# Optimization experiments

Measured on AMD Instinct MI355X. Metric: run time of the kernel, lower is better.

## Reference

```python
import jax, jax.numpy as jnp
import numpy as np

N, T, J, NB = 2048, 81, 16, 15
D_ATT, HEADS, SEQ, D_LIN, NOISE = 48, 6, 31, 256, 45
BN_EPS, LN_EPS, SLOPE = 1e-5, 1e-6, 0.01

# Human3.6M 16-joint skeleton bone (parent, child) pairs
_BONES = [(0,1),(1,2),(2,3),(0,4),(4,5),(5,6),(0,7),(7,8),(8,9),(9,10),(8,11),(11,12),(12,13),(8,14),(14,15)]
BONES_P = np.array([p for p, c in _BONES])
BONES_C = np.array([c for p, c in _BONES])
_parent = {c: p for p, c in _BONES}
_bone_of = {c: i for i, (p, c) in enumerate(_BONES)}
_M = np.zeros((NB, J), np.float32)  # M[i,j]=1 iff bone i lies on root->joint j chain
for j in range(1, J):
    jj = j
    while jj != 0:
        _M[_bone_of[jj], j] = 1.0
        jj = _parent[jj]
M_BONE2POSE = jnp.asarray(_M)
FIXED_MASK = jnp.ones((NB,), jnp.float32).at[jnp.array([6, 7])].set(0.0)  # torso bones kept fixed


def _layer_norm(t, a, b):
    mean = t.mean(-1, keepdims=True)
    # torch.std default is unbiased (ddof=1); module divides by (std + eps)
    std = jnp.sqrt(((t - mean) ** 2).sum(-1, keepdims=True) / (t.shape[-1] - 1))
    return a * (t - mean) / (std + LN_EPS) + b


def _leaky(x):
    return jnp.where(x >= 0, x, SLOPE * x)


def _axis_angle_to_matrix(v):
    # Rodrigues: v (..., 3) axis-angle -> (..., 3, 3)
    theta = jnp.linalg.norm(v, axis=-1, keepdims=True)
    k = v / jnp.maximum(theta, 1e-8)
    c = jnp.cos(theta)[..., None]
    s = jnp.sin(theta)[..., None]
    kx, ky, kz = k[..., 0], k[..., 1], k[..., 2]
    z = jnp.zeros_like(kx)
    K = jnp.stack([jnp.stack([z, -kz, ky], -1),
                   jnp.stack([kz, z, -kx], -1),
                   jnp.stack([-ky, kx, z], -1)], -2)
    kk = k[..., :, None] * k[..., None, :]
    return c * jnp.eye(3, dtype=v.dtype) + s * K + (1 - c) * kk


def setup_inputs() -> dict:
    key = jax.random.key(0)
    ks = jax.random.split(key, 12)
    w = lambda k, shape, scale=0.05: jax.random.normal(k, shape, jnp.float32) * scale
    return {
        'inputs_3d': jax.random.normal(ks[0], (N, 1, T, J, 3), jnp.float32),
        'noise': jax.random.normal(ks[1], (N, NOISE), jnp.float32),
        'enc_w': w(ks[2], (D_ATT, 3)), 'enc_b': jnp.zeros((D_ATT,), jnp.float32),
        'enc_bn_g': jnp.ones((D_ATT,), jnp.float32), 'enc_bn_b': jnp.zeros((D_ATT,), jnp.float32),
        'ln_a': jnp.ones((D_ATT,), jnp.float32), 'ln_b': jnp.zeros((D_ATT,), jnp.float32),
        'wq': w(ks[3], (D_ATT, D_ATT)), 'bq': jnp.zeros((D_ATT,), jnp.float32),
        'wk': w(ks[4], (D_ATT, D_ATT)), 'bk': jnp.zeros((D_ATT,), jnp.float32),
        'wv': w(ks[5], (D_ATT, D_ATT)), 'bv': jnp.zeros((D_ATT,), jnp.float32),
        'wo': w(ks[6], (D_ATT, D_ATT)), 'bo': jnp.zeros((D_ATT,), jnp.float32),
        'w1': w(ks[7], (D_LIN, SEQ * D_ATT)), 'b1': jnp.zeros((D_LIN,), jnp.float32),
        'bn1_g': jnp.ones((D_LIN,), jnp.float32), 'bn1_b': jnp.zeros((D_LIN,), jnp.float32),
        'w2': w(ks[8], (NB * 4, D_LIN)), 'b2': w(ks[9], (NB * 4,), 0.1),
    }


def reference(inputs_3d, noise, enc_w, enc_b, enc_bn_g, enc_bn_b, ln_a, ln_b,
              wq, bq, wk, bk, wv, bv, wo, bo, w1, b1, bn1_g, bn1_b, w2, b2):
    x5 = inputs_3d[:, 0]                                  # (n, T, 16, 3)
    root = x5[:, :, :1, :]
    x = x5 - root                                         # root-centered
    bvec = x[..., BONES_C, :] - x[..., BONES_P, :]        # (n, T, 15, 3)
    blen = jnp.linalg.norm(bvec, axis=-1, keepdims=True)
    bunit = bvec / blen
    n, t_len = x.shape[0], x.shape[1]
    mid = (t_len - 1) // 2

    x_ = x[:, mid].reshape(n, -1)                         # (n, 48)
    y = jnp.concatenate([x_, noise], axis=-1).reshape(n, SEQ, 3)
    # Conv1d(k=1) == per-token linear; BatchNorm eval (running mean 0, var 1); Dropout off
    y = jax.nn.relu((y @ enc_w.T + enc_b) * enc_bn_g / jnp.sqrt(1.0 + BN_EPS) + enc_bn_b)

    # tiny 6-head self-attention with pre-LayerNorm and residual
    h = _layer_norm(y, ln_a, ln_b)
    d = D_ATT // HEADS
    q = (h @ wq.T + bq).reshape(n, SEQ, HEADS, d).transpose(0, 2, 1, 3)
    k = (h @ wk.T + bk).reshape(n, SEQ, HEADS, d).transpose(0, 2, 1, 3)
    v = (h @ wv.T + bv).reshape(n, SEQ, HEADS, d).transpose(0, 2, 1, 3)
    probs = jax.nn.softmax(jnp.einsum('nhqd,nhkd->nhqk', q, k) / (d ** 0.5), axis=-1)
    ctx = jnp.einsum('nhqk,nhkd->nhqd', probs, v).transpose(0, 2, 1, 3).reshape(n, SEQ, D_ATT)
    y = y + (ctx @ wo.T + bo)

    y = y.reshape(n, -1)                                  # (n, 1488)
    y = _leaky((y @ w1.T + b1) * bn1_g / jnp.sqrt(1.0 + BN_EPS) + bn1_b)
    y = _leaky(y @ w2.T + b2).reshape(n, NB, 4)           # (n, 15, 4)

    axis = y[..., :3]
    axis = axis / jnp.linalg.norm(axis, axis=-1, keepdims=True)
    theta = y[..., 3:4] / t_len                           # (n, 15, 1)
    t_idx = jnp.arange(t_len, dtype=y.dtype)              # (T,)
    vaa = axis[:, None] * (theta[:, None] * t_idx[None, :, None, None])  # (n, T, 15, 3)
    R = _axis_angle_to_matrix(vaa)                        # (n, T, 15, 3, 3)
    mod_unit = jnp.einsum('ntbij,ntbj->ntbi', R, bunit)
    mask = FIXED_MASK[None, None, :, None]
    mod_unit = mod_unit * mask + bunit * (1 - mask)
    ba_diff = 1 - jnp.sum(mod_unit * bunit, axis=-1)      # (n, T, 15)
    mod_bone = mod_unit * blen
    out = jnp.einsum('ntbc,bj->ntjc', mod_bone, M_BONE2POSE) + root  # (n, T, 16, 3)
    return out, ba_diff
```

## Files before the change

kernel.cpp:

```cpp
#include <hip/hip_runtime.h>
#include <math.h>

#define NS   2048
#define TL   81
#define NBN  15
#define DA   48
#define SQL  31
#define KD   1488
#define DL   256
#define MID  40
#define SWLD 52

#define INV_SQRT_BN 0.99999500003749969f
#define SCALE_ATT   0.35355339059327373f

__global__ __launch_bounds__(256)
void attn_kernel(const float* __restrict__ x5, const float* __restrict__ noise,
                 const float* __restrict__ enc_w, const float* __restrict__ enc_b,
                 const float* __restrict__ enc_g, const float* __restrict__ enc_bb,
                 const float* __restrict__ ln_a, const float* __restrict__ ln_b,
                 const float* __restrict__ wq, const float* __restrict__ bq,
                 const float* __restrict__ wk, const float* __restrict__ bk,
                 const float* __restrict__ wv, const float* __restrict__ bv,
                 const float* __restrict__ wo, const float* __restrict__ bo,
                 float* __restrict__ y2)
{
    __shared__ float s93[96];
    __shared__ __align__(16) float sy[32*SWLD];
    __shared__ __align__(16) float sh[32*SWLD];
    __shared__ __align__(16) float sW[3*48*SWLD];
    __shared__ __align__(16) float sQKV[32*148];
    __shared__ float smean[32], sinv[32];

    const int tid = threadIdx.x;
    const int n = blockIdx.x;

    if (tid < 93) {
        float v;
        if (tid < 48) {
            const float* base = x5 + ((size_t)n*TL + MID)*48;
            v = base[tid] - base[tid % 3];
        } else {
            v = noise[(size_t)n*45 + (tid-48)];
        }
        s93[tid] = v;
    }
    #pragma unroll
    for (int l=0; l<9; l++){
        int idx = tid + l*256;
        int f = idx/48, c = idx - f*48;
        int o = f*SWLD + c;
        sW[o]             = wq[idx];
        sW[48*SWLD  + o]  = wk[idx];
        sW[96*SWLD  + o]  = wv[idx];
    }
    __syncthreads();

    for (int idx=tid; idx<SQL*DA; idx+=256){
        int s = idx/48, f = idx - s*48;
        float a = enc_b[f]
                + s93[s*3+0]*enc_w[f*3+0]
                + s93[s*3+1]*enc_w[f*3+1]
                + s93[s*3+2]*enc_w[f*3+2];
        float v = a * (enc_g[f]*INV_SQRT_BN) + enc_bb[f];
        sy[s*SWLD+f] = fmaxf(v, 0.0f);
    }
    __syncthreads();

    if (tid < SQL){
        float m = 0.f;
        for (int f=0; f<48; f++) m += sy[tid*SWLD+f];
        m *= (1.0f/48.0f);
        float vs = 0.f;
        for (int f=0; f<48; f++){ float d = sy[tid*SWLD+f]-m; vs += d*d; }
        float sd = sqrtf(vs * (1.0f/47.0f));
        smean[tid] = m;
        sinv[tid]  = 1.0f/(sd + 1e-6f);
    }
    __syncthreads();

    for (int idx=tid; idx<SQL*DA; idx+=256){
        int s = idx/48, f = idx - s*48;
        sh[s*SWLD+f] = ln_a[f]*(sy[s*SWLD+f]-smean[s])*sinv[s] + ln_b[f];
    }
    __syncthreads();

    if (tid < 192){
        const int sg  = tid/24;
        const int rem = tid - sg*24;
        const int arr = rem >> 3;
        const int fg  = rem & 7;
        const int f0  = fg*6;
        const int s0  = sg*4;
        const float* wb = sW + arr*48*SWLD + f0*SWLD;
        const float* hb = sh + s0*SWLD;
        float acc[4][6];
        #pragma unroll
        for (int j=0;j<4;j++)
            #pragma unroll
            for (int i=0;i<6;i++) acc[j][i]=0.f;
        for (int cc=0; cc<12; cc++){
            const int c0 = 4*((fg + cc) % 12);
            float4 h0 = *(const float4*)(hb + 0*SWLD + c0);
            float4 h1 = *(const float4*)(hb + 1*SWLD + c0);
            float4 h2 = *(const float4*)(hb + 2*SWLD + c0);
            float4 h3 = *(const float4*)(hb + 3*SWLD + c0);
            #pragma unroll
            for (int i=0;i<6;i++){
                float4 w = *(const float4*)(wb + i*SWLD + c0);
                acc[0][i] += h0.x*w.x + h0.y*w.y + h0.z*w.z + h0.w*w.w;
                acc[1][i] += h1.x*w.x + h1.y*w.y + h1.z*w.z + h1.w*w.w;
                acc[2][i] += h2.x*w.x + h2.y*w.y + h2.z*w.z + h2.w*w.w;
                acc[3][i] += h3.x*w.x + h3.y*w.y + h3.z*w.z + h3.w*w.w;
            }
        }
        const float* bias = (arr==0)? bq : (arr==1? bk : bv);
        #pragma unroll
        for (int i=0;i<6;i++){
            float b = bias[f0+i];
            int col = arr*48 + f0 + i;
            sQKV[(s0+0)*148 + col] = acc[0][i] + b;
            sQKV[(s0+1)*148 + col] = acc[1][i] + b;
            sQKV[(s0+2)*148 + col] = acc[2][i] + b;
            sQKV[(s0+3)*148 + col] = acc[3][i] + b;
        }
    }
    __syncthreads();

    #pragma unroll
    for (int l=0; l<9; l++){
        int idx = tid + l*256;
        sW[(idx/48)*SWLD + (idx%48)] = wo[idx];
    }
    if (tid < 186){
        const int hd = tid/31, qi = tid - (tid/31)*31;
        const float4 q0 = *(const float4*)(sQKV + qi*148 + hd*8);
        const float4 q1 = *(const float4*)(sQKV + qi*148 + hd*8 + 4);
        float sc[31]; float mx = -1e30f;
        for (int ki=0; ki<31; ki++){
            const float4 k0 = *(const float4*)(sQKV + ki*148 + 48 + hd*8);
            const float4 k1 = *(const float4*)(sQKV + ki*148 + 48 + hd*8 + 4);
            float d = q0.x*k0.x + q0.y*k0.y + q0.z*k0.z + q0.w*k0.w
                    + q1.x*k1.x + q1.y*k1.y + q1.z*k1.z + q1.w*k1.w;
            d *= SCALE_ATT;
            sc[ki] = d; mx = fmaxf(mx, d);
        }
        float ssum = 0.f;
        for (int ki=0; ki<31; ki++){ float e = expf(sc[ki]-mx); sc[ki]=e; ssum += e; }
        float rin = 1.0f/ssum;
        float4 c0 = {0,0,0,0}, c1 = {0,0,0,0};
        for (int ki=0; ki<31; ki++){
            float p = sc[ki];
            const float4 v0 = *(const float4*)(sQKV + ki*148 + 96 + hd*8);
            const float4 v1 = *(const float4*)(sQKV + ki*148 + 96 + hd*8 + 4);
            c0.x += p*v0.x; c0.y += p*v0.y; c0.z += p*v0.z; c0.w += p*v0.w;
            c1.x += p*v1.x; c1.y += p*v1.y; c1.z += p*v1.z; c1.w += p*v1.w;
        }
        float* cb = sh + qi*SWLD + hd*8;
        float4 o0, o1;
        o0.x=c0.x*rin; o0.y=c0.y*rin; o0.z=c0.z*rin; o0.w=c0.w*rin;
        o1.x=c1.x*rin; o1.y=c1.y*rin; o1.z=c1.z*rin; o1.w=c1.w*rin;
        *(float4*)(cb)   = o0;
        *(float4*)(cb+4) = o1;
    }
    __syncthreads();

    if (tid < 192){
        const int sg = tid/12;
        const int fg = tid - sg*12;
        const int f0 = fg*4;
        const float* wb = sW + f0*SWLD;
        const float* cb = sh + sg*2*SWLD;
        float a0[4]={0,0,0,0}, a1[4]={0,0,0,0};
        for (int cc=0; cc<12; cc++){
            const int c0 = 4*((fg + cc) % 12);
            float4 x0 = *(const float4*)(cb + c0);
            float4 x1 = *(const float4*)(cb + SWLD + c0);
            #pragma unroll
            for (int i=0;i<4;i++){
                float4 w = *(const float4*)(wb + i*SWLD + c0);
                a0[i] += x0.x*w.x + x0.y*w.y + x0.z*w.z + x0.w*w.w;
                a1[i] += x1.x*w.x + x1.y*w.y + x1.z*w.z + x1.w*w.w;
            }
        }
        {
            int s = sg*2;
            if (s < 31){
                float* dst = y2 + (size_t)n*KD + s*48 + f0;
                const float* yb = sy + s*SWLD + f0;
                #pragma unroll
                for (int i=0;i<4;i++) dst[i] = yb[i] + a0[i] + bo[f0+i];
            }
        }
        {
            int s = sg*2+1;
            if (s < 31){
                float* dst = y2 + (size_t)n*KD + s*48 + f0;
                const float* yb = sy + s*SWLD + f0;
                #pragma unroll
                for (int i=0;i<4;i++) dst[i] = yb[i] + a1[i] + bo[f0+i];
            }
        }
    }
}

#define KSP 6
#define KPS 248
#define KCH 8

__global__ __launch_bounds__(256)
void gemm1_kernel(const float* __restrict__ y2, const float* __restrict__ w1,
                  float* __restrict__ y3p)
{
    __shared__ __align__(16) float sB[KCH*256];
    __shared__ __align__(16) float sA[KCH*20];
    const int tid = threadIdx.x;
    const int bx = blockIdx.x;
    const int m0 = (bx & 127) * 16;
    const int split = bx >> 7;
    const int ks0 = split * KPS;
    const int c0 = (tid & 15)*4 + (tid >> 6)*64;
    const int r0 = ((tid >> 4) & 3)*4;

    const int bn = tid >> 1;
    const int bg = (tid & 1)*4;
    const int ar = tid >> 1;
    const int ag = (tid & 1)*4;

    float acc[4][4];
    #pragma unroll
    for (int i=0;i<4;i++)
        #pragma unroll
        for (int j=0;j<4;j++) acc[i][j]=0.f;

    for (int ch=0; ch<31; ch++){
        const int k0 = ks0 + ch*KCH;
        float4 b0v = *(const float4*)(w1 + (size_t)bn*KD        + k0 + bg);
        float4 b1v = *(const float4*)(w1 + (size_t)(bn+128)*KD  + k0 + bg);
        float4 av;
        if (tid < 32) av = *(const float4*)(y2 + (size_t)(m0+ar)*KD + k0 + ag);
        __syncthreads();
        sB[(bg+0)*256 + bn] = b0v.x;  sB[(bg+1)*256 + bn] = b0v.y;
        sB[(bg+2)*256 + bn] = b0v.z;  sB[(bg+3)*256 + bn] = b0v.w;
        sB[(bg+0)*256 + bn+128] = b1v.x;  sB[(bg+1)*256 + bn+128] = b1v.y;
        sB[(bg+2)*256 + bn+128] = b1v.z;  sB[(bg+3)*256 + bn+128] = b1v.w;
        if (tid < 32){
            sA[(ag+0)*20 + ar] = av.x;  sA[(ag+1)*20 + ar] = av.y;
            sA[(ag+2)*20 + ar] = av.z;  sA[(ag+3)*20 + ar] = av.w;
        }
        __syncthreads();
        #pragma unroll
        for (int kk=0; kk<KCH; kk++){
            float4 b = *(const float4*)(sB + kk*256 + c0);
            float4 a = *(const float4*)(sA + kk*20 + r0);
            acc[0][0] += a.x*b.x; acc[0][1] += a.x*b.y; acc[0][2] += a.x*b.z; acc[0][3] += a.x*b.w;
            acc[1][0] += a.y*b.x; acc[1][1] += a.y*b.y; acc[1][2] += a.y*b.z; acc[1][3] += a.y*b.w;
            acc[2][0] += a.z*b.x; acc[2][1] += a.z*b.y; acc[2][2] += a.z*b.z; acc[2][3] += a.z*b.w;
            acc[3][0] += a.w*b.x; acc[3][1] += a.w*b.y; acc[3][2] += a.w*b.z; acc[3][3] += a.w*b.w;
        }
    }

    float* dst = y3p + (size_t)split*NS*DL;
    #pragma unroll
    for (int i=0;i<4;i++){
        float4 v; v.x=acc[i][0]; v.y=acc[i][1]; v.z=acc[i][2]; v.w=acc[i][3];
        *(float4*)(dst + (size_t)(m0+r0+i)*DL + c0) = v;
    }
}

__global__ __launch_bounds__(256)
void head_kernel(const float* __restrict__ y3p, const float* __restrict__ w2,
                 const float* __restrict__ b2, const float* __restrict__ b1,
                 const float* __restrict__ g1, const float* __restrict__ bb1,
                 float* __restrict__ at)
{
    __shared__ float swc[64*60];
    __shared__ __align__(16) float sy3[8*256];
    __shared__ float sy4[8*61];
    const int tid = threadIdx.x;
    const int n0 = blockIdx.x * 8;

    #pragma unroll
    for (int l=0;l<2;l++){
        int idx = tid + l*256;
        int s = idx >> 6, i4 = (idx & 63) << 2;
        const float* src = y3p + (size_t)(n0+s)*256 + i4;
        float4 v = *(const float4*)(src);
        #pragma unroll
        for (int sl=1; sl<6; sl++){
            float4 p = *(const float4*)(src + (size_t)sl*NS*DL);
            v.x += p.x; v.y += p.y; v.z += p.z; v.w += p.w;
        }
        const float4 vb = *(const float4*)(b1 + i4);
        const float4 vg = *(const float4*)(g1 + i4);
        const float4 vs = *(const float4*)(bb1 + i4);
        v.x = (v.x + vb.x)*(vg.x*INV_SQRT_BN) + vs.x;  v.x = v.x>=0.f? v.x : 0.01f*v.x;
        v.y = (v.y + vb.y)*(vg.y*INV_SQRT_BN) + vs.y;  v.y = v.y>=0.f? v.y : 0.01f*v.y;
        v.z = (v.z + vb.z)*(vg.z*INV_SQRT_BN) + vs.z;  v.z = v.z>=0.f? v.z : 0.01f*v.z;
        v.w = (v.w + vb.w)*(vg.w*INV_SQRT_BN) + vs.w;  v.w = v.w>=0.f? v.w : 0.01f*v.w;
        *(float4*)(sy3 + s*256 + i4) = v;
    }

    float acc[2]; int ss[2], mm[2];
    #pragma unroll
    for (int l=0;l<2;l++){
        int uu = tid + l*256;
        ss[l]=0; mm[l]=0; acc[l]=0.f;
        if (uu < 480){ ss[l]=uu/60; mm[l]=uu-ss[l]*60; acc[l]=b2[mm[l]]; }
    }

    for (int ch=0; ch<4; ch++){
        const int i0 = ch*64;
        __syncthreads();
        #pragma unroll
        for (int l=0;l<15;l++){
            int idx = tid + l*256;
            int m = idx >> 6, io = idx & 63;
            swc[io*60 + m] = w2[(size_t)m*256 + i0 + io];
        }
        __syncthreads();
        #pragma unroll
        for (int l=0;l<2;l++){
            int uu = tid + l*256;
            if (uu < 480){
                const float* yy = sy3 + ss[l]*256 + i0;
                float a = acc[l];
                #pragma unroll 8
                for (int io=0; io<64; io++) a += yy[io]*swc[io*60 + mm[l]];
                acc[l] = a;
            }
        }
    }
    __syncthreads();
    #pragma unroll
    for (int l=0;l<2;l++){
        int uu = tid + l*256;
        if (uu < 480){
            float a = acc[l];
            sy4[ss[l]*61 + mm[l]] = a>=0.f? a : 0.01f*a;
        }
    }
    __syncthreads();
    if (tid < 120){
        int s = tid/15, b = tid - s*15;
        const float* y4 = sy4 + s*61 + b*4;
        float ax=y4[0], ay=y4[1], az=y4[2], th=y4[3];
        float nr = sqrtf(ax*ax+ay*ay+az*az);
        float4 o;
        o.x = ax/nr; o.y = ay/nr; o.z = az/nr; o.w = th/81.0f;
        *(float4*)(at + (size_t)(n0+s)*60 + b*4) = o;
    }
}

__global__ __launch_bounds__(256)
void pose_kernel(const float* __restrict__ x5, const float* __restrict__ at,
                 float* __restrict__ out)
{
    const int gid = blockIdx.x*256 + threadIdx.x;
    if (gid >= NS*TL) return;
    const int n = gid / TL;
    const int t = gid - n*TL;
    const float ft = (float)t;

    float4 pv[12];
    {
        const float4* src = (const float4*)(x5 + (size_t)gid*48);
        #pragma unroll
        for (int i=0;i<12;i++) pv[i] = src[i];
    }
    float* p = (float*)pv;
    const float4* ab = (const float4*)(at + (size_t)n*60);

    float4 posv[12];
    float* pos = (float*)posv;
    pos[0]=p[0]; pos[1]=p[1]; pos[2]=p[2];
    float ba[15];

    const int PJ[15] = {0,1,2,0,4,5,0,7,8,9,8,11,12,8,14};
    const int CJ[15] = {1,2,3,4,5,6,7,8,9,10,11,12,13,14,15};

    #pragma unroll
    for (int b=0;b<15;b++){
        const int pj = PJ[b], cj = CJ[b];
        float bx = p[cj*3+0]-p[pj*3+0];
        float by = p[cj*3+1]-p[pj*3+1];
        float bz = p[cj*3+2]-p[pj*3+2];
        float bl = sqrtf(bx*bx+by*by+bz*bz);
        float ux = bx/bl, uy = by/bl, uz = bz/bl;
        float mx, my, mz;
        if (b==6 || b==7){
            mx=ux; my=uy; mz=uz;
        } else {
            float4 a = ab[b];
            float ang = a.w * ft;
            float cs = __cosf(ang), sn = __sinf(ang);
            float kd = a.x*ux + a.y*uy + a.z*uz;
            float cx = a.y*uz - a.z*uy;
            float cy = a.z*ux - a.x*uz;
            float cz = a.x*uy - a.y*ux;
            float oc = (1.0f-cs)*kd;
            mx = ux*cs + cx*sn + a.x*oc;
            my = uy*cs + cy*sn + a.y*oc;
            mz = uz*cs + cz*sn + a.z*oc;
        }
        ba[b] = 1.0f - (mx*ux+my*uy+mz*uz);
        pos[cj*3+0] = pos[pj*3+0] + mx*bl;
        pos[cj*3+1] = pos[pj*3+1] + my*bl;
        pos[cj*3+2] = pos[pj*3+2] + mz*bl;
    }

    {
        float4* dst = (float4*)(out + (size_t)gid*48);
        #pragma unroll
        for (int i=0;i<12;i++) dst[i] = posv[i];
    }
    {
        float* bd = out + (size_t)NS*TL*48 + (size_t)gid*15;
        #pragma unroll
        for (int b=0;b<15;b++) bd[b] = ba[b];
    }
}

extern "C" void kernel_launch(void* const* d_in, const int* in_sizes, int n_in,
                              void* d_out, int out_size, void* d_ws, size_t ws_size,
                              hipStream_t stream)
{
    const float* x5    = (const float*)d_in[0];
    const float* noise = (const float*)d_in[1];
    const float* enc_w = (const float*)d_in[2];
    const float* enc_b = (const float*)d_in[3];
    const float* enc_g = (const float*)d_in[4];
    const float* enc_bb= (const float*)d_in[5];
    const float* ln_a  = (const float*)d_in[6];
    const float* ln_b  = (const float*)d_in[7];
    const float* wq = (const float*)d_in[8];
    const float* bq = (const float*)d_in[9];
    const float* wk = (const float*)d_in[10];
    const float* bk = (const float*)d_in[11];
    const float* wv = (const float*)d_in[12];
    const float* bv = (const float*)d_in[13];
    const float* wo = (const float*)d_in[14];
    const float* bo = (const float*)d_in[15];
    const float* w1 = (const float*)d_in[16];
    const float* b1 = (const float*)d_in[17];
    const float* g1 = (const float*)d_in[18];
    const float* bb1= (const float*)d_in[19];
    const float* w2 = (const float*)d_in[20];
    const float* b2 = (const float*)d_in[21];
    float* out = (float*)d_out;

    float* ws = (float*)d_ws;
    float* y2 = ws;
    float* at = y2 + (size_t)NS*KD;

    float* y3p = out;

    attn_kernel<<<NS, 256, 0, stream>>>(x5, noise, enc_w, enc_b, enc_g, enc_bb,
                                        ln_a, ln_b, wq,bq,wk,bk,wv,bv,wo,bo, y2);
    gemm1_kernel<<<128*KSP, 256, 0, stream>>>(y2, w1, y3p);
    head_kernel<<<NS/8, 256, 0, stream>>>(y3p, w2, b2, b1, g1, bb1, at);
    pose_kernel<<<(NS*TL+255)/256, 256, 0, stream>>>(x5, at, out);

    (void)in_sizes; (void)n_in; (void)out_size; (void)ws_size;
}
```

Before: 236.3 us.

## Drop shared-memory staging in gemm1; load A and B tiles directly per thread

The split-K GEMM no longer stages W1 and activation chunks through LDS with two barriers per chunk. Each thread now reads its own 4 rows of A and 4 rows of W1 straight from global memory as float4 and accumulates dot products in registers. This removes the barriers and LDS traffic but gives up cross-thread reuse: each W1 row is read by many threads, so the kernel leans on L1/L2 cache. The strided row access pattern also coalesces poorly within a wavefront.

Measured after the change: 307.5 us. 30.1% more time.

```diff
diff --git a/kernel.cpp b/kernel.cpp
--- a/kernel.cpp
+++ b/kernel.cpp
@@ -212,8 +212,6 @@
 void gemm1_kernel(const float* __restrict__ y2, const float* __restrict__ w1,
                   float* __restrict__ y3p)
 {
-    __shared__ __align__(16) float sB[KCH*256];
-    __shared__ __align__(16) float sA[KCH*20];
     const int tid = threadIdx.x;
     const int bx = blockIdx.x;
     const int m0 = (bx & 127) * 16;
@@ -222,10 +220,8 @@
     const int c0 = (tid & 15)*4 + (tid >> 6)*64;
     const int r0 = ((tid >> 4) & 3)*4;
 
-    const int bn = tid >> 1;
-    const int bg = (tid & 1)*4;
-    const int ar = tid >> 1;
-    const int ag = (tid & 1)*4;
+    const float* arow = y2 + (size_t)(m0+r0)*KD + ks0;
+    const float* brow = w1 + (size_t)c0*KD + ks0;
 
     float acc[4][4];
     #pragma unroll
@@ -234,29 +230,27 @@
         for (int j=0;j<4;j++) acc[i][j]=0.f;
 
     for (int ch=0; ch<31; ch++){
-        const int k0 = ks0 + ch*KCH;
-        float4 b0v = *(const float4*)(w1 + (size_t)bn*KD        + k0 + bg);
-        float4 b1v = *(const float4*)(w1 + (size_t)(bn+128)*KD  + k0 + bg);
-        float4 av;
-        if (tid < 32) av = *(const float4*)(y2 + (size_t)(m0+ar)*KD + k0 + ag);
-        __syncthreads();
-        sB[(bg+0)*256 + bn] = b0v.x;  sB[(bg+1)*256 + bn] = b0v.y;
-        sB[(bg+2)*256 + bn] = b0v.z;  sB[(bg+3)*256 + bn] = b0v.w;
-        sB[(bg+0)*256 + bn+128] = b1v.x;  sB[(bg+1)*256 + bn+128] = b1v.y;
-        sB[(bg+2)*256 + bn+128] = b1v.z;  sB[(bg+3)*256 + bn+128] = b1v.w;
-        if (tid < 32){
-            sA[(ag+0)*20 + ar] = av.x;  sA[(ag+1)*20 + ar] = av.y;
-            sA[(ag+2)*20 + ar] = av.z;  sA[(ag+3)*20 + ar] = av.w;
-        }
-        __syncthreads();
-        #pragma unroll
-        for (int kk=0; kk<KCH; kk++){
-            float4 b = *(const float4*)(sB + kk*256 + c0);
-            float4 a = *(const float4*)(sA + kk*20 + r0);
-            acc[0][0] += a.x*b.x; acc[0][1] += a.x*b.y; acc[0][2] += a.x*b.z; acc[0][3] += a.x*b.w;
-            acc[1][0] += a.y*b.x; acc[1][1] += a.y*b.y; acc[1][2] += a.y*b.z; acc[1][3] += a.y*b.w;
-            acc[2][0] += a.z*b.x; acc[2][1] += a.z*b.y; acc[2][2] += a.z*b.z; acc[2][3] += a.z*b.w;
-            acc[3][0] += a.w*b.x; acc[3][1] += a.w*b.y; acc[3][2] += a.w*b.z; acc[3][3] += a.w*b.w;
+        const int k0 = ch*KCH;
+        float4 a0[4], a1[4], b0[4], b1[4];
+        #pragma unroll
+        for (int i=0;i<4;i++){
+            a0[i] = *(const float4*)(arow + (size_t)i*KD + k0);
+            a1[i] = *(const float4*)(arow + (size_t)i*KD + k0 + 4);
+        }
+        #pragma unroll
+        for (int j=0;j<4;j++){
+            b0[j] = *(const float4*)(brow + (size_t)j*KD + k0);
+            b1[j] = *(const float4*)(brow + (size_t)j*KD + k0 + 4);
+        }
+        #pragma unroll
+        for (int i=0;i<4;i++){
+            #pragma unroll
+            for (int j=0;j<4;j++){
+                acc[i][j] += a0[i].x*b0[j].x + a0[i].y*b0[j].y
+                           + a0[i].z*b0[j].z + a0[i].w*b0[j].w
+                           + a1[i].x*b1[j].x + a1[i].y*b1[j].y
+                           + a1[i].z*b1[j].z + a1[i].w*b1[j].w;
+            }
         }
     }
 
```
